# Performance work log

Hardware: AMD Instinct MI355X
Metric: run time of the kernel (lower is better)

The kernel has to match this reference:

```python
import jax, jax.numpy as jnp
import numpy as np

B, T, N = 8, 512, 64        # batch, seq_len, enc_in
E, H, P = 128, 256, 96      # embed_size, hidden_size, pred_len
LAMBDA = 0.001              # softshrink sparsity threshold
SCALE = 0.02


def _leaky(h):
    return jnp.where(h >= 0, h, 0.01 * h)


def _softshrink(y):
    return jnp.where(y > LAMBDA, y - LAMBDA, jnp.where(y < -LAMBDA, y + LAMBDA, jnp.zeros_like(y)))


def setup_inputs() -> dict:
    key = jax.random.key(0)
    ks = jax.random.split(key, 16)
    f32 = jnp.float32
    d = {
        "x": jax.random.normal(ks[0], (B, T, N), f32),
        "emb": jax.random.normal(ks[1], (1, E), f32),
        # MLP (embed_size -> hidden -> embed_size), stored as [in, out]
        "w1": SCALE * jax.random.normal(ks[2], (E, H), f32),
        "b1": SCALE * jax.random.normal(ks[3], (H,), f32),
        "w2": SCALE * jax.random.normal(ks[4], (H, E), f32),
        "b2": SCALE * jax.random.normal(ks[5], (E,), f32),
        # MLP_time (seq_len -> hidden -> seq_len)
        "tw1": SCALE * jax.random.normal(ks[6], (T, H), f32),
        "tb1": SCALE * jax.random.normal(ks[7], (H,), f32),
        "tw2": SCALE * jax.random.normal(ks[8], (H, T), f32),
        "tb2": SCALE * jax.random.normal(ks[9], (T,), f32),
        # fc (seq_len*embed -> hidden -> pred_len)
        "fw1": SCALE * jax.random.normal(ks[10], (T * E, H), f32),
        "fb1": SCALE * jax.random.normal(ks[11], (H,), f32),
        "fw2": SCALE * jax.random.normal(ks[12], (H, P), f32),
        "fb2": SCALE * jax.random.normal(ks[13], (P,), f32),
    }
    return d


def reference(x, emb, w1, b1, w2, b2, tw1, tb1, tw2, tb2, fw1, fb1, fw2, fb2):
    # x: [B, T, N]
    x_noD = jnp.transpose(x, (0, 2, 1))            # [B, N, T]
    xe = x_noD[..., None] * emb                    # tokenEmb -> [B, N, T, E]
    bias = xe + x_noD[..., None]

    # NorMLP_temporal: rfft over time, shared MLP on real/imag, softshrink, irfft
    xf = jnp.fft.rfft(xe, axis=2, norm="ortho")   # [B, N, T//2+1, E] complex64

    def mlp(z):
        return _leaky(z @ w1 + b1) @ w2 + b2

    yr = _softshrink(mlp(xf.real))
    yi = _softshrink(mlp(xf.imag))
    y = jax.lax.complex(yr, yi)
    xt = jnp.fft.irfft(y, n=T, axis=2, norm="ortho")  # [B, N, T, E]

    # NorMLP_temporal_WO_freq: MLP_time over last (time) dim of x_noD
    xn = _leaky(x_noD @ tw1 + tb1) @ tw2 + tb2        # [B, N, T]

    out = xt + xn[..., None] + bias                   # use_bias = 1

    flat = out.reshape(B, N, T * E)
    h = _leaky(flat @ fw1 + fb1) @ fw2 + fb2          # [B, N, P]
    return jnp.transpose(h, (0, 2, 1))                # [B, P, N]
```

## Files before the change

kernel.cpp:

```cpp
#include <hip/hip_runtime.h>
#include <hip/hip_bf16.h>


typedef unsigned int uint;
typedef unsigned short ushort_t;
typedef __attribute__((ext_vector_type(4))) float f32x4;
typedef __attribute__((ext_vector_type(8))) short short8;

#define LAMBDA_ 0.001f
#define RSQRT512 0.044194173824159220f

__device__ __forceinline__ ushort_t f2bf(float f) {
    uint u = __float_as_uint(f);
    uint r = (u + 0x7FFFu + ((u >> 16) & 1u)) >> 16;
    return (ushort_t)r;
}
__device__ __forceinline__ ushort_t f2bf_hw(float f) {
    union { __hip_bfloat16 h; ushort_t u; } c;
    c.h = __float2bfloat16(f);
    return c.u;
}
__device__ __forceinline__ float bf2f(ushort_t v) { return __uint_as_float(((uint)v) << 16); }
__device__ __forceinline__ float leaky_(float v) { return v >= 0.f ? v : 0.01f * v; }

__device__ __forceinline__ void gload_lds16(const ushort_t* g, ushort_t* l) {
    __builtin_amdgcn_global_load_lds((const __attribute__((address_space(1))) void*)g,
                                     (__attribute__((address_space(3))) void*)l, 16, 0, 0);
}

__global__ __launch_bounds__(256) void k_pre_plus(const float* __restrict__ x, const float* __restrict__ tw1,
                                                  const float* __restrict__ tw2, const float* __restrict__ fw1,
                                                  const float* __restrict__ emb, const float* __restrict__ w1,
                                                  const float* __restrict__ b1,
                                                  ushort_t* __restrict__ A1cat, ushort_t* __restrict__ B1cat,
                                                  ushort_t* __restrict__ Wt, ushort_t* __restrict__ tw2_bf,
                                                  ushort_t* __restrict__ fw1T,
                                                  float* __restrict__ u_g, int* __restrict__ idxs_g,
                                                  float* __restrict__ bpkey_g) {
    __shared__ float tile[64 * 65];
    __shared__ float key_s[256];
    __shared__ int idx_s[256];
    int bid = blockIdx.x;
    int tid = threadIdx.x;
    if (bid < 3072) {
        int region = bid >> 10;
        int id = ((bid & 1023) << 8) + tid;
        int a = id >> 9, c = id & 511;
        if (region == 0) {
            int f = (a <= 256) ? a : (a - 256);
            int m = (c * f) & 511;
            float ang = (float)m * (6.283185307179586f / 512.0f);
            float v = ((a <= 256) ? cosf(ang) : -sinf(ang)) * RSQRT512;
            ushort_t hi = f2bf(v);
            ushort_t lo = f2bf(v - bf2f(hi));
            size_t row = (size_t)a * 1536;
            B1cat[row + c] = hi;
            B1cat[row + 512 + c] = hi;
            B1cat[row + 1024 + c] = lo;
        } else if (region == 1) {
            int f = (a <= 256) ? a : (a - 256);
            int m = (c * f) & 511;
            float ang = (float)m * (6.283185307179586f / 512.0f);
            float v = ((a <= 256) ? cosf(ang) : -sinf(ang)) * RSQRT512;
            float sc = (a == 0 || a == 256) ? 1.0f : 2.0f;
            Wt[id] = f2bf(v * sc);
        } else {
            if ((bid & 1023) < 512) tw2_bf[id] = f2bf(tw2[id]);
        }
    } else if (bid < 3104) {
        int b = bid - 3072;
        int t0 = (b & 7) << 6, h0 = (b >> 3) << 6;
        float (*t64)[65] = (float(*)[65])tile;
        for (int i = 0; i < 16; ++i) {
            int idx = tid + i * 256;
            int r = idx >> 6, cc = idx & 63;
            t64[r][cc] = tw1[(size_t)(t0 + r) * 256 + h0 + cc];
        }
        __syncthreads();
        for (int i = 0; i < 16; ++i) {
            int idx = tid + i * 256;
            int rr = idx >> 6, cc2 = idx & 63;
            float v = t64[cc2][rr];
            ushort_t hi = f2bf(v);
            ushort_t lo = f2bf(v - bf2f(hi));
            size_t row = (size_t)(512 + h0 + rr) * 1536;
            int t = t0 + cc2;
            B1cat[row + t] = hi;
            B1cat[row + 512 + t] = hi;
            B1cat[row + 1024 + t] = lo;
        }
    } else if (bid < 3360) {
        int b = bid - 3104;
        int bb = b >> 5;
        int rem = b & 31;
        int t0 = (rem >> 1) << 5;
        int n0 = (rem & 1) << 5;
        int tx = tid & 31, ty = tid >> 5;
        float (*t32)[33] = (float(*)[33])tile;
        for (int i = 0; i < 4; ++i) {
            int tt = ty * 4 + i;
            t32[tt][tx] = x[(size_t)(bb * 512 + t0 + tt) * 64 + n0 + tx];
        }
        __syncthreads();
        for (int i = 0; i < 4; ++i) {
            int nn = ty * 4 + i;
            float v = t32[tx][nn];
            ushort_t hi = f2bf(v);
            ushort_t lo = f2bf(v - bf2f(hi));
            size_t row = (size_t)(bb * 64 + n0 + nn) * 1536;
            int t = t0 + tx;
            A1cat[row + t] = hi;
            A1cat[row + 512 + t] = lo;
            A1cat[row + 1024 + t] = hi;
        }
    } else if (bid < 7456) {
        int b = bid - 3360;
        int e  = b & 127;
        int hb = (b >> 7) & 3;
        int tt = b >> 9;
        int t0 = tt << 6, h0 = hb << 6;
        float (*t64)[65] = (float(*)[65])tile;
        for (int i = 0; i < 4; ++i) {
            int idx = tid + i * 256;
            int r = idx >> 4, c4 = idx & 15;
            const float* src = fw1 + ((size_t)(t0 + r) * 128 + e) * 256 + h0 + c4 * 4;
            float4 v = *(const float4*)src;
            t64[r][c4 * 4 + 0] = v.x;
            t64[r][c4 * 4 + 1] = v.y;
            t64[r][c4 * 4 + 2] = v.z;
            t64[r][c4 * 4 + 3] = v.w;
        }
        __syncthreads();
        for (int p = 0; p < 2; ++p) {
            int idx = tid + p * 256;
            int hh = idx >> 3, tg = idx & 7;
            short8 o;
            for (int j = 0; j < 8; ++j) o[j] = (short)f2bf(t64[tg * 8 + j][hh]);
            *(short8*)(fw1T + ((size_t)(h0 + hh) * 128 + e) * 512 + t0 + tg * 8) = o;
        }
    } else {
        float acc = 0.f;
#pragma unroll 8
        for (int e = 0; e < 128; ++e) acc += emb[e] * w1[e * 256 + tid];
        u_g[tid] = acc;
        float bb0 = b1[tid];
        key_s[tid] = (acc == 0.f) ? INFINITY : (-bb0 / acc);
        idx_s[tid] = tid;
        __syncthreads();
        for (int k = 2; k <= 256; k <<= 1) {
            for (int j = k >> 1; j > 0; j >>= 1) {
                int ixj = tid ^ j;
                if (ixj > tid) {
                    bool up = ((tid & k) == 0);
                    float a0 = key_s[tid], a1 = key_s[ixj];
                    if ((a0 > a1) == up) {
                        key_s[tid] = a1; key_s[ixj] = a0;
                        int t0 = idx_s[tid]; idx_s[tid] = idx_s[ixj]; idx_s[ixj] = t0;
                    }
                }
                __syncthreads();
            }
        }
        bpkey_g[tid] = key_s[tid];
        idxs_g[tid] = idx_s[tid];
    }
}

__global__ __launch_bounds__(256) void k_mid(const ushort_t* __restrict__ fw1T, const float* __restrict__ emb,
                                             const float* __restrict__ tb2,
                                             ushort_t* __restrict__ B1cat, ushort_t* __restrict__ F1sbf,
                                             float* __restrict__ p2v,
                                             const float* __restrict__ u_g, const float* __restrict__ b1,
                                             const float* __restrict__ w2, const float* __restrict__ b2,
                                             const int* __restrict__ idxs_g,
                                             ushort_t* __restrict__ Atab, ushort_t* __restrict__ Btab) {
    __shared__ float embs[128];
    __shared__ float red[256];
    __shared__ float sA[256], sB[256];
    int bid = blockIdx.x;
    int tid = threadIdx.x;
    if (bid < 256) {
        int h = bid;
        if (tid < 128) embs[tid] = 1.f + emb[tid];
        __syncthreads();
        int t2 = tid * 2;
        const ushort_t* base = fw1T + ((size_t)h << 16) + t2;
        float as0 = 0.f, as1 = 0.f, ae0 = 0.f, ae1 = 0.f;
#pragma unroll 4
        for (int e = 0; e < 128; ++e) {
            uint v = *(const uint*)(base + (size_t)e * 512);
            float v0 = bf2f((ushort_t)(v & 0xffff));
            float v1 = bf2f((ushort_t)(v >> 16));
            float w = embs[e];
            as0 += v0; as1 += v1;
            ae0 += w * v0; ae1 += w * v1;
        }
        *(uint*)(F1sbf + (size_t)h * 512 + t2) = (uint)f2bf(as0) | ((uint)f2bf(as1) << 16);
        ushort_t hi0 = f2bf(ae0), hi1 = f2bf(ae1);
        ushort_t lo0 = f2bf(ae0 - bf2f(hi0)), lo1 = f2bf(ae1 - bf2f(hi1));
        size_t row = (size_t)(768 + h) * 1536;
        uint hpk = (uint)hi0 | ((uint)hi1 << 16);
        *(uint*)(B1cat + row + t2) = hpk;
        *(uint*)(B1cat + row + 512 + t2) = hpk;
        *(uint*)(B1cat + row + 1024 + t2) = (uint)lo0 | ((uint)lo1 << 16);
        red[tid] = tb2[t2] * as0 + tb2[t2 + 1] * as1;
        __syncthreads();
        for (int off = 128; off > 0; off >>= 1) {
            if (tid < off) red[tid] += red[tid + off];
            __syncthreads();
        }
        if (tid == 0) p2v[h] = red[0];
    } else {
        int e = bid - 256, r = tid;
        float uu0 = u_g[r], bb0 = b1[r];
        float w0 = w2[r * 128 + e];
        float c = (uu0 < 0.f || (uu0 == 0.f && bb0 >= 0.f)) ? 1.0f : 0.01f;
        float bA = c * uu0 * w0, bB = c * bb0 * w0;
        int h = idxs_g[r];
        float uu = u_g[h], bb = b1[h];
        float w = w2[h * 128 + e];
        float sgn = (uu > 0.f) ? 0.99f : -0.99f;
        float dA = sgn * uu * w, dB = sgn * bb * w;
        sA[r] = bA; sB[r] = bB;
        __syncthreads();
        for (int off = 128; off > 0; off >>= 1) {
            if (r < off) { sA[r] += sA[r + off]; sB[r] += sB[r + off]; }
            __syncthreads();
        }
        float baseA = sA[0], baseB = sB[0] + b2[e];
        __syncthreads();
        sA[r] = dA; sB[r] = dB;
        __syncthreads();
        for (int off = 1; off < 256; off <<= 1) {
            float vA = (r >= off) ? sA[r - off] : 0.f;
            float vB = (r >= off) ? sB[r - off] : 0.f;
            __syncthreads();
            sA[r] += vA; sB[r] += vB;
            __syncthreads();
        }
        if (r == 0) { Atab[e] = f2bf(baseA); Btab[e] = f2bf(baseB); }
        Atab[(r + 1) * 128 + e] = f2bf(baseA + sA[r]);
        Btab[(r + 1) * 128 + e] = f2bf(baseB + sB[r]);
    }
}

__global__ __launch_bounds__(256) void k_g1p2(const ushort_t* __restrict__ A, const ushort_t* __restrict__ Bm,
                                              float* __restrict__ partialG,
                                              const ushort_t* __restrict__ tw2bf, const ushort_t* __restrict__ F1sbf,
                                              ushort_t* __restrict__ P2T) {
    __shared__ ushort_t As[128 * 72];
    __shared__ ushort_t Bs[128 * 72];
    int tid = threadIdx.x;
    int lane = tid & 63, wid = tid >> 6;
    int wr = wid >> 1, wc = wid & 1;
    int bid = blockIdx.x;
    f32x4 acc[4][4] = {};
    if (bid < 256) {
        int kch = bid & 7, tilei = bid >> 3;
        int nt = tilei & 7, mt = tilei >> 3;
        int m0 = mt * 128, n0 = nt * 128;
        for (int kt = 0; kt < 3; ++kt) {
            int kb = kch * 192 + kt * 64;
            __syncthreads();
            {
                uint4 va[4], vb[4];
                for (int i = 0; i < 4; ++i) {
                    int q = tid + i * 256;
                    int row = q >> 3, kcc = (q & 7) << 3;
                    va[i] = *(const uint4*)(A + (size_t)(m0 + row) * 1536 + kb + kcc);
                    vb[i] = *(const uint4*)(Bm + (size_t)(n0 + row) * 1536 + kb + kcc);
                }
                for (int i = 0; i < 4; ++i) {
                    int q = tid + i * 256;
                    int row = q >> 3, kcc = (q & 7) << 3;
                    *(uint4*)&As[row * 72 + kcc] = va[i];
                    *(uint4*)&Bs[row * 72 + kcc] = vb[i];
                }
            }
            __syncthreads();
            for (int ks = 0; ks < 2; ++ks) {
                short8 a[4], b[4];
                int kk = ks * 32 + (lane >> 4) * 8;
                for (int mi = 0; mi < 4; ++mi)
                    a[mi] = *(const short8*)&As[(wr * 64 + mi * 16 + (lane & 15)) * 72 + kk];
                for (int ni = 0; ni < 4; ++ni)
                    b[ni] = *(const short8*)&Bs[(wc * 64 + ni * 16 + (lane & 15)) * 72 + kk];
                for (int mi = 0; mi < 4; ++mi)
                    for (int ni = 0; ni < 4; ++ni)
                        acc[mi][ni] = __builtin_amdgcn_mfma_f32_16x16x32_bf16(a[mi], b[ni], acc[mi][ni], 0, 0, 0);
            }
        }
        float* pbase = partialG + (size_t)kch * 524288;
        int mb0 = m0 + wr * 64 + ((lane >> 4) << 2);
        int nb0 = n0 + wc * 64 + (lane & 15);
        for (int mi = 0; mi < 4; ++mi)
            for (int ni = 0; ni < 4; ++ni) {
                int mbase = mb0 + mi * 16;
                int n = nb0 + ni * 16;
                for (int r = 0; r < 4; ++r)
                    pbase[(size_t)(mbase + r) * 1024 + n] = acc[mi][ni][r];
            }
    } else {
        int b2i = bid - 256;
        int nt = b2i & 1, mt = b2i >> 1;
        int m0 = mt * 128, n0 = nt * 128;
        for (int kt = 0; kt < 8; ++kt) {
            int kb = kt * 64;
            __syncthreads();
            {
                uint4 va[4], vb[4];
                for (int i = 0; i < 4; ++i) {
                    int q = tid + i * 256;
                    int row = q >> 3, kcc = (q & 7) << 3;
                    va[i] = *(const uint4*)(tw2bf + (size_t)(m0 + row) * 512 + kb + kcc);
                    vb[i] = *(const uint4*)(F1sbf + (size_t)(n0 + row) * 512 + kb + kcc);
                }
                for (int i = 0; i < 4; ++i) {
                    int q = tid + i * 256;
                    int row = q >> 3, kcc = (q & 7) << 3;
                    *(uint4*)&As[row * 72 + kcc] = va[i];
                    *(uint4*)&Bs[row * 72 + kcc] = vb[i];
                }
            }
            __syncthreads();
            for (int ks = 0; ks < 2; ++ks) {
                short8 a[4], b[4];
                int kk = ks * 32 + (lane >> 4) * 8;
                for (int mi = 0; mi < 4; ++mi)
                    a[mi] = *(const short8*)&As[(wr * 64 + mi * 16 + (lane & 15)) * 72 + kk];
                for (int ni = 0; ni < 4; ++ni)
                    b[ni] = *(const short8*)&Bs[(wc * 64 + ni * 16 + (lane & 15)) * 72 + kk];
                for (int mi = 0; mi < 4; ++mi)
                    for (int ni = 0; ni < 4; ++ni)
                        acc[mi][ni] = __builtin_amdgcn_mfma_f32_16x16x32_bf16(a[mi], b[ni], acc[mi][ni], 0, 0, 0);
            }
        }
        int mb0 = m0 + wr * 64 + ((lane >> 4) << 2);
        int nb0 = n0 + wc * 64 + (lane & 15);
        for (int mi = 0; mi < 4; ++mi)
            for (int ni = 0; ni < 4; ++ni) {
                int mbase = mb0 + mi * 16;
                int n = nb0 + ni * 16;
                ushort4 o;
                o.x = f2bf(acc[mi][ni][0]);
                o.y = f2bf(acc[mi][ni][1]);
                o.z = f2bf(acc[mi][ni][2]);
                o.w = f2bf(acc[mi][ni][3]);
                *(ushort4*)(P2T + (size_t)n * 256 + mbase) = o;
            }
    }
}

__global__ __launch_bounds__(512) void k_gemm0r(const ushort_t* __restrict__ A, const ushort_t* __restrict__ Bm,
                                                ushort_t* __restrict__ M2T,
                                                const float* __restrict__ partialG, const float* __restrict__ tb1,
                                                float* __restrict__ s, ushort_t* __restrict__ hl,
                                                float* __restrict__ h2c) {
    __shared__ ushort_t As[2][128 * 64];
    __shared__ ushort_t Bs[2][128 * 64];
    int tid = threadIdx.x;
    int bid = blockIdx.x;
    if (bid >= 1024) {
        int id = (bid - 1024) * 512 + tid;
        int m = id >> 10, n = id & 1023;
        float acc = 0.f;
#pragma unroll
        for (int kc = 0; kc < 8; ++kc)
            acc += partialG[(size_t)kc * 524288 + id];
        if (n < 512) s[(size_t)m * 512 + n] = acc;
        else if (n < 768) hl[(size_t)m * 256 + (n - 512)] = f2bf(leaky_(acc + tb1[n - 512]));
        else h2c[(size_t)m * 256 + (n - 768)] = acc;
        return;
    }
    int lane = tid & 63, wid = tid >> 6;
    int wr = wid >> 2, wc = wid & 3;
    int xx = bid & 7, y = bid >> 3;
    int mt = y & 3;
    int nt = ((y >> 2) << 3) | xx;
    int m0 = mt * 128, n0 = nt * 128;
    int lrow = lane >> 3;
    int sg = (lane & 7) ^ lrow;
    auto issue = [&](int kt, int buf) {
        int kb = kt * 64;
        for (int i = 0; i < 2; ++i) {
            int rbase = wid * 16 + i * 8;
            gload_lds16(A + (size_t)(m0 + rbase + lrow) * 512 + kb + sg * 8, &As[buf][wid * 1024 + i * 512]);
            gload_lds16(Bm + (size_t)(n0 + rbase + lrow) * 512 + kb + sg * 8, &Bs[buf][wid * 1024 + i * 512]);
        }
    };
    f32x4 acc[4][2] = {};
    issue(0, 0);
    __syncthreads();
    int cur = 0;
    for (int kt = 0; kt < 8; ++kt) {
        int nxt = cur ^ 1;
        if (kt + 1 < 8) issue(kt + 1, nxt);
        __builtin_amdgcn_s_setprio(1);
        for (int ks = 0; ks < 2; ++ks) {
            short8 a[4], b[2];
            int sl = ks * 4 + (lane >> 4);
            for (int mi = 0; mi < 4; ++mi) {
                int row = wr * 64 + mi * 16 + (lane & 15);
                a[mi] = *(const short8*)&As[cur][row * 64 + ((sl ^ (row & 7)) << 3)];
            }
            for (int ni = 0; ni < 2; ++ni) {
                int row = wc * 32 + ni * 16 + (lane & 15);
                b[ni] = *(const short8*)&Bs[cur][row * 64 + ((sl ^ (row & 7)) << 3)];
            }
            for (int mi = 0; mi < 4; ++mi)
                for (int ni = 0; ni < 2; ++ni)
                    acc[mi][ni] = __builtin_amdgcn_mfma_f32_16x16x32_bf16(a[mi], b[ni], acc[mi][ni], 0, 0, 0);
        }
        __builtin_amdgcn_s_setprio(0);
        __syncthreads();
        cur = nxt;
    }
    ushort_t* cstage = &As[0][0];
    for (int mi = 0; mi < 4; ++mi) {
        int ml = wr * 64 + mi * 16 + ((lane >> 4) << 2);
        for (int ni = 0; ni < 2; ++ni) {
            int nl = wc * 32 + ni * 16 + (lane & 15);
            for (int r = 0; r < 4; ++r) {
                int row = ml + r;
                cstage[row * 128 + (nl ^ ((row & 7) << 4))] = f2bf(acc[mi][ni][r]);
            }
        }
    }
    __syncthreads();
    short8* d8 = (short8*)(M2T + ((size_t)(n0 >> 7) << 16) + (size_t)m0 * 128);
    for (int i = 0; i < 4; ++i) {
        int p = tid + i * 512;
        int row = p >> 4;
        int col0 = (p & 15) * 8;
        d8[p] = *(const short8*)&cstage[row * 128 + (col0 ^ ((row & 7) << 4))];
    }
}

__global__ __launch_bounds__(512) void k_gemm1(const float* __restrict__ s,
                                               const ushort_t* __restrict__ Atab, const ushort_t* __restrict__ Btab,
                                               const float* __restrict__ bpkey,
                                               const ushort_t* __restrict__ Bm,
                                               float* __restrict__ partial) {
    __shared__ ushort_t As[2][128 * 64];
    __shared__ ushort_t Bs[2][256 * 64];
    __shared__ float sv_s[1024];
    __shared__ ushort_t r_s[1024];
    __shared__ float bp_s[256];
    int tid = threadIdx.x;
    int lane = tid & 63, wid = tid >> 6;
    int wr = wid >> 2, wc = wid & 3;
    int bid = blockIdx.x;
    int xcd = bid & 7, j = bid >> 3;
    int kcl = j & 7, mt = j >> 3;
    int kc = xcd * 8 + kcl;
    int m0 = mt * 128;
    int k0 = kc * 1024;
    if (tid < 256) bp_s[tid] = bpkey[tid];
    __syncthreads();
    {
        int row = tid >> 2, j2 = (tid & 3) * 2;
        float2 sv2 = *(const float2*)(s + (size_t)(m0 + row) * 512 + kc * 8 + j2);
        float svv[2] = {sv2.x, sv2.y};
        for (int q = 0; q < 2; ++q) {
            float sv = svv[q];
            int lo = 0, hi = 256;
            while (lo < hi) { int mid = (lo + hi) >> 1; if (bp_s[mid] <= sv) lo = mid + 1; else hi = mid; }
            sv_s[row * 8 + j2 + q] = sv;
            r_s[row * 8 + j2 + q] = (ushort_t)lo;
        }
    }
    __syncthreads();

    int lrow = lane >> 3;
    int sg = (lane & 7) ^ lrow;
    auto issueB = [&](int kt, int buf) {
        int kb = k0 + kt * 64;
        for (int i = 0; i < 4; ++i) {
            int rbase = wid * 32 + i * 8;
            gload_lds16(Bm + (size_t)(rbase + lrow) * 65536 + kb + sg * 8, &Bs[buf][wid * 2048 + i * 512]);
        }
    };
    short8 ta[2], tb[2];
    float svr[2];
    auto gather = [&](int kt) {
        int kl = kt >> 1;
        for (int i = 0; i < 2; ++i) {
            int q = tid + i * 512;
            int row = q >> 3, slot = q & 7;
            int e0 = ((kt & 1) << 6) + slot * 8;
            int r = r_s[row * 8 + kl];
            svr[i] = sv_s[row * 8 + kl];
            ta[i] = *(const short8*)(Atab + r * 128 + e0);
            tb[i] = *(const short8*)(Btab + r * 128 + e0);
        }
    };
    auto cookwrite = [&](int buf) {
        for (int i = 0; i < 2; ++i) {
            int q = tid + i * 512;
            int row = q >> 3, slot = q & 7;
            float sv = svr[i];
            short8 o;
            for (int jj = 0; jj < 8; ++jj) {
                float y = fmaf(sv, bf2f((ushort_t)ta[i][jj]), bf2f((ushort_t)tb[i][jj]));
                y = y - fminf(fmaxf(y, -LAMBDA_), LAMBDA_);
                o[jj] = (short)f2bf_hw(y);
            }
            *(short8*)&As[buf][row * 64 + ((slot ^ (row & 7)) << 3)] = o;
        }
    };

    f32x4 acc[4][4] = {};
    issueB(0, 0);
    gather(0);
    cookwrite(0);
    __syncthreads();
    int cur = 0;
    for (int kt = 0; kt < 16; ++kt) {
        int nxt = cur ^ 1;
        if (kt + 1 < 16) { issueB(kt + 1, nxt); gather(kt + 1); }
        __builtin_amdgcn_s_setprio(1);
        for (int ks = 0; ks < 2; ++ks) {
            short8 a[4], b[4];
            int sl = ks * 4 + (lane >> 4);
            for (int mi = 0; mi < 4; ++mi) {
                int row = wr * 64 + mi * 16 + (lane & 15);
                a[mi] = *(const short8*)&As[cur][row * 64 + ((sl ^ (row & 7)) << 3)];
            }
            for (int ni = 0; ni < 4; ++ni) {
                int row = wc * 64 + ni * 16 + (lane & 15);
                b[ni] = *(const short8*)&Bs[cur][row * 64 + ((sl ^ (row & 7)) << 3)];
            }
            for (int mi = 0; mi < 4; ++mi)
                for (int ni = 0; ni < 4; ++ni)
                    acc[mi][ni] = __builtin_amdgcn_mfma_f32_16x16x32_bf16(a[mi], b[ni], acc[mi][ni], 0, 0, 0);
        }
        __builtin_amdgcn_s_setprio(0);
        if (kt + 1 < 16) cookwrite(nxt);
        __syncthreads();
        cur = nxt;
    }
    int mb0 = m0 + wr * 64 + ((lane >> 4) << 2);
    int nb0 = wc * 64 + (lane & 15);
    float* pbase = partial + (size_t)kc * 131072;
    for (int mi = 0; mi < 4; ++mi)
        for (int ni = 0; ni < 4; ++ni) {
            int mbase = mb0 + mi * 16;
            int n = nb0 + ni * 16;
            for (int r = 0; r < 4; ++r)
                pbase[(size_t)(mbase + r) * 256 + n] = acc[mi][ni][r];
        }
}

__global__ __launch_bounds__(128) void k_final(const float* __restrict__ partial, const ushort_t* __restrict__ hl,
                                               const ushort_t* __restrict__ P2T, const float* __restrict__ p2v,
                                               const float* __restrict__ h2c, const float* __restrict__ fb1,
                                               const float* __restrict__ fw2, const float* __restrict__ fb2,
                                               float* __restrict__ out) {
    __shared__ float a_s[256];
    __shared__ float hl_s[256];
    int bn = blockIdx.x;
    int tid = threadIdx.x;
    {
        uint v = *(const uint*)(hl + (size_t)bn * 256 + tid * 2);
        hl_s[tid * 2] = bf2f((ushort_t)(v & 0xffff));
        hl_s[tid * 2 + 1] = bf2f((ushort_t)(v >> 16));
    }
    __syncthreads();
    for (int p = 0; p < 2; ++p) {
        int i = tid + p * 128;
        float acc = p2v[i] + h2c[(size_t)bn * 256 + i] + fb1[i];
#pragma unroll 8
        for (int kc = 0; kc < 64; ++kc)
            acc += partial[((size_t)kc * 512 + bn) * 256 + i];
        const ushort_t* prow = P2T + (size_t)i * 256;
#pragma unroll 4
        for (int jb = 0; jb < 32; ++jb) {
            short8 pv = *(const short8*)(prow + jb * 8);
            for (int j8 = 0; j8 < 8; ++j8)
                acc += hl_s[jb * 8 + j8] * bf2f((ushort_t)pv[j8]);
        }
        a_s[i] = leaky_(acc);
    }
    __syncthreads();
    if (tid < 96) {
        float acc = fb2[tid];
        for (int hh = 0; hh < 256; ++hh)
            acc += a_s[hh] * fw2[hh * 96 + tid];
        int b = bn >> 6, n = bn & 63;
        out[(size_t)(b * 96 + tid) * 64 + n] = acc;
    }
}

extern "C" void kernel_launch(void* const* d_in, const int* in_sizes, int n_in,
                              void* d_out, int out_size, void* d_ws, size_t ws_size,
                              hipStream_t stream) {
    const float* x   = (const float*)d_in[0];
    const float* emb = (const float*)d_in[1];
    const float* w1  = (const float*)d_in[2];
    const float* b1  = (const float*)d_in[3];
    const float* w2  = (const float*)d_in[4];
    const float* b2  = (const float*)d_in[5];
    const float* tw1 = (const float*)d_in[6];
    const float* tb1 = (const float*)d_in[7];
    const float* tw2 = (const float*)d_in[8];
    const float* tb2 = (const float*)d_in[9];
    const float* fw1 = (const float*)d_in[10];
    const float* fb1 = (const float*)d_in[11];
    const float* fw2 = (const float*)d_in[12];
    const float* fb2 = (const float*)d_in[13];
    float* out = (float*)d_out;

    char* W = (char*)d_ws;
    size_t off = 0;
    auto take = [&](size_t bytes) { size_t r = off; off += (bytes + 255) & ~(size_t)255; return r; };
    ushort_t* fw1T  = (ushort_t*)(W + take(33554432));
    ushort_t* M2T   = (ushort_t*)(W + take(33554432));
    float* partial  = (float*)(W + take(64 * 512 * 256 * 4));
    float* partialG = (float*)(W + take(8 * 512 * 1024 * 4));
    ushort_t* A1cat = (ushort_t*)(W + take(512 * 1536 * 2));
    ushort_t* B1cat = (ushort_t*)(W + take(1024 * 1536 * 2));
    ushort_t* Wt    = (ushort_t*)(W + take(512 * 512 * 2));
    ushort_t* tw2bf = (ushort_t*)(W + take(256 * 512 * 2));
    ushort_t* F1sbf = (ushort_t*)(W + take(256 * 512 * 2));
    float* sbuf     = (float*)(W + take(512 * 512 * 4));
    ushort_t* hlbuf = (ushort_t*)(W + take(512 * 256 * 2));
    float* h2c      = (float*)(W + take(512 * 256 * 4));
    ushort_t* P2T   = (ushort_t*)(W + take(256 * 256 * 2));
    float* p2v      = (float*)(W + take(256 * 4));
    ushort_t* Atab  = (ushort_t*)(W + take(257 * 128 * 2));
    ushort_t* Btab  = (ushort_t*)(W + take(257 * 128 * 2));
    float* bpkey    = (float*)(W + take(256 * 4));
    float* u_g      = (float*)(W + take(256 * 4));
    int* idxs_g     = (int*)(W + take(256 * 4));
    (void)ws_size; (void)in_sizes; (void)n_in; (void)out_size;

    k_pre_plus<<<7457, 256, 0, stream>>>(x, tw1, tw2, fw1, emb, w1, b1,
                                         A1cat, B1cat, Wt, tw2bf, fw1T, u_g, idxs_g, bpkey);
    k_mid<<<384, 256, 0, stream>>>(fw1T, emb, tb2, B1cat, F1sbf, p2v,
                                   u_g, b1, w2, b2, idxs_g, Atab, Btab);
    k_g1p2<<<260, 256, 0, stream>>>(A1cat, B1cat, partialG, tw2bf, F1sbf, P2T);
    k_gemm0r<<<2048, 512, 0, stream>>>(Wt, fw1T, M2T, partialG, tb1, sbuf, hlbuf, h2c);
    k_gemm1<<<256, 512, 0, stream>>>(sbuf, Atab, Btab, bpkey, M2T, partial);
    k_final<<<512, 128, 0, stream>>>(partial, hlbuf, P2T, p2v, h2c, fb1, fw2, fb2, out);
}
```

Baseline: 141.3 us.

## Merge three GEMM stages into one launch and fold split-K reduction into consumers

Merges the two independent GEMM kernels (the M2T GEMM and the split-K/P2 GEMMs) into a single 512-thread launch that shares a double-buffered, swizzled global-to-LDS tile loop. The separate reduction pass that summed the 8 split-K partials into s, hl and h2c buffers is removed. That reduction now happens inside k_gemm1 and k_final, which read partialG directly. This saves one kernel launch, an intermediate round trip through memory and a serialization point. The cost is redundant partial-sum reads in the consumer kernels and smaller per-warp tiles for the split-K GEMMs.

```diff
diff --git a/kernel.cpp b/kernel.cpp
--- a/kernel.cpp
+++ b/kernel.cpp
@@ -26,6 +26,50 @@
 __device__ __forceinline__ void gload_lds16(const ushort_t* g, ushort_t* l) {
     __builtin_amdgcn_global_load_lds((const __attribute__((address_space(1))) void*)g,
                                      (__attribute__((address_space(3))) void*)l, 16, 0, 0);
+}
+
+__device__ __forceinline__ void tile_loop512(const ushort_t* __restrict__ A, int lda,
+                                             const ushort_t* __restrict__ Bm, int ldb,
+                                             int m0, int n0, int k0, int kIters,
+                                             f32x4 (&acc)[4][2],
+                                             ushort_t (&As)[2][128 * 64], ushort_t (&Bs)[2][128 * 64],
+                                             int tid, int lane, int wid, int wr, int wc) {
+    int lrow = lane >> 3;
+    int sg = (lane & 7) ^ lrow;
+    auto issue = [&](int kt, int buf) {
+        int kb = k0 + kt * 64;
+        for (int i = 0; i < 2; ++i) {
+            int rbase = wid * 16 + i * 8;
+            gload_lds16(A + (size_t)(m0 + rbase + lrow) * lda + kb + sg * 8, &As[buf][wid * 1024 + i * 512]);
+            gload_lds16(Bm + (size_t)(n0 + rbase + lrow) * ldb + kb + sg * 8, &Bs[buf][wid * 1024 + i * 512]);
+        }
+    };
+    issue(0, 0);
+    __syncthreads();
+    int cur = 0;
+    for (int kt = 0; kt < kIters; ++kt) {
+        int nxt = cur ^ 1;
+        if (kt + 1 < kIters) issue(kt + 1, nxt);
+        __builtin_amdgcn_s_setprio(1);
+        for (int ks = 0; ks < 2; ++ks) {
+            short8 a[4], b[2];
+            int sl = ks * 4 + (lane >> 4);
+            for (int mi = 0; mi < 4; ++mi) {
+                int row = wr * 64 + mi * 16 + (lane & 15);
+                a[mi] = *(const short8*)&As[cur][row * 64 + ((sl ^ (row & 7)) << 3)];
+            }
+            for (int ni = 0; ni < 2; ++ni) {
+                int row = wc * 32 + ni * 16 + (lane & 15);
+                b[ni] = *(const short8*)&Bs[cur][row * 64 + ((sl ^ (row & 7)) << 3)];
+            }
+            for (int mi = 0; mi < 4; ++mi)
+                for (int ni = 0; ni < 2; ++ni)
+                    acc[mi][ni] = __builtin_amdgcn_mfma_f32_16x16x32_bf16(a[mi], b[ni], acc[mi][ni], 0, 0, 0);
+        }
+        __builtin_amdgcn_s_setprio(0);
+        __syncthreads();
+        cur = nxt;
+    }
 }
 
 __global__ __launch_bounds__(256) void k_pre_plus(const float* __restrict__ x, const float* __restrict__ tw1,
@@ -244,101 +288,69 @@
     }
 }
 
-__global__ __launch_bounds__(256) void k_g1p2(const ushort_t* __restrict__ A, const ushort_t* __restrict__ Bm,
+__global__ __launch_bounds__(512) void k_big3(const ushort_t* __restrict__ Wt, const ushort_t* __restrict__ fw1T,
+                                              ushort_t* __restrict__ M2T,
+                                              const ushort_t* __restrict__ A1cat, const ushort_t* __restrict__ B1cat,
                                               float* __restrict__ partialG,
                                               const ushort_t* __restrict__ tw2bf, const ushort_t* __restrict__ F1sbf,
                                               ushort_t* __restrict__ P2T) {
-    __shared__ ushort_t As[128 * 72];
-    __shared__ ushort_t Bs[128 * 72];
+    __shared__ ushort_t As[2][128 * 64];
+    __shared__ ushort_t Bs[2][128 * 64];
     int tid = threadIdx.x;
     int lane = tid & 63, wid = tid >> 6;
-    int wr = wid >> 1, wc = wid & 1;
+    int wr = wid >> 2, wc = wid & 3;
     int bid = blockIdx.x;
-    f32x4 acc[4][4] = {};
-    if (bid < 256) {
-        int kch = bid & 7, tilei = bid >> 3;
+    f32x4 acc[4][2] = {};
+    if (bid < 1024) {
+        int xx = bid & 7, y = bid >> 3;
+        int mt = y & 3;
+        int nt = ((y >> 2) << 3) | xx;
+        int m0 = mt * 128, n0 = nt * 128;
+        tile_loop512(Wt, 512, fw1T, 512, m0, n0, 0, 8, acc, As, Bs, tid, lane, wid, wr, wc);
+        ushort_t* cstage = &As[0][0];
+        for (int mi = 0; mi < 4; ++mi) {
+            int ml = wr * 64 + mi * 16 + ((lane >> 4) << 2);
+            for (int ni = 0; ni < 2; ++ni) {
+                int nl = wc * 32 + ni * 16 + (lane & 15);
+                for (int r = 0; r < 4; ++r) {
+                    int row = ml + r;
+                    cstage[row * 128 + (nl ^ ((row & 7) << 4))] = f2bf(acc[mi][ni][r]);
+                }
+            }
+        }
+        __syncthreads();
+        short8* d8 = (short8*)(M2T + ((size_t)(n0 >> 7) << 16) + (size_t)m0 * 128);
+        for (int i = 0; i < 4; ++i) {
+            int p = tid + i * 512;
+            int row = p >> 4;
+            int col0 = (p & 15) * 8;
+            d8[p] = *(const short8*)&cstage[row * 128 + (col0 ^ ((row & 7) << 4))];
+        }
+    } else if (bid < 1280) {
+        int b = bid - 1024;
+        int kch = b & 7, tilei = b >> 3;
         int nt = tilei & 7, mt = tilei >> 3;
         int m0 = mt * 128, n0 = nt * 128;
-        for (int kt = 0; kt < 3; ++kt) {
-            int kb = kch * 192 + kt * 64;
-            __syncthreads();
-            {
-                uint4 va[4], vb[4];
-                for (int i = 0; i < 4; ++i) {
-                    int q = tid + i * 256;
-                    int row = q >> 3, kcc = (q & 7) << 3;
-                    va[i] = *(const uint4*)(A + (size_t)(m0 + row) * 1536 + kb + kcc);
-                    vb[i] = *(const uint4*)(Bm + (size_t)(n0 + row) * 1536 + kb + kcc);
-                }
-                for (int i = 0; i < 4; ++i) {
-                    int q = tid + i * 256;
-                    int row = q >> 3, kcc = (q & 7) << 3;
-                    *(uint4*)&As[row * 72 + kcc] = va[i];
-                    *(uint4*)&Bs[row * 72 + kcc] = vb[i];
-                }
-            }
-            __syncthreads();
-            for (int ks = 0; ks < 2; ++ks) {
-                short8 a[4], b[4];
-                int kk = ks * 32 + (lane >> 4) * 8;
-                for (int mi = 0; mi < 4; ++mi)
-                    a[mi] = *(const short8*)&As[(wr * 64 + mi * 16 + (lane & 15)) * 72 + kk];
-                for (int ni = 0; ni < 4; ++ni)
-                    b[ni] = *(const short8*)&Bs[(wc * 64 + ni * 16 + (lane & 15)) * 72 + kk];
-                for (int mi = 0; mi < 4; ++mi)
-                    for (int ni = 0; ni < 4; ++ni)
-                        acc[mi][ni] = __builtin_amdgcn_mfma_f32_16x16x32_bf16(a[mi], b[ni], acc[mi][ni], 0, 0, 0);
-            }
-        }
+        tile_loop512(A1cat, 1536, B1cat, 1536, m0, n0, kch * 192, 3, acc, As, Bs, tid, lane, wid, wr, wc);
         float* pbase = partialG + (size_t)kch * 524288;
         int mb0 = m0 + wr * 64 + ((lane >> 4) << 2);
-        int nb0 = n0 + wc * 64 + (lane & 15);
+        int nb0 = n0 + wc * 32 + (lane & 15);
         for (int mi = 0; mi < 4; ++mi)
-            for (int ni = 0; ni < 4; ++ni) {
+            for (int ni = 0; ni < 2; ++ni) {
                 int mbase = mb0 + mi * 16;
                 int n = nb0 + ni * 16;
                 for (int r = 0; r < 4; ++r)
                     pbase[(size_t)(mbase + r) * 1024 + n] = acc[mi][ni][r];
             }
     } else {
-        int b2i = bid - 256;
-        int nt = b2i & 1, mt = b2i >> 1;
+        int b = bid - 1280;
+        int nt = b & 1, mt = b >> 1;
         int m0 = mt * 128, n0 = nt * 128;
-        for (int kt = 0; kt < 8; ++kt) {
-            int kb = kt * 64;
-            __syncthreads();
-            {
-                uint4 va[4], vb[4];
-                for (int i = 0; i < 4; ++i) {
-                    int q = tid + i * 256;
-                    int row = q >> 3, kcc = (q & 7) << 3;
-                    va[i] = *(const uint4*)(tw2bf + (size_t)(m0 + row) * 512 + kb + kcc);
-                    vb[i] = *(const uint4*)(F1sbf + (size_t)(n0 + row) * 512 + kb + kcc);
-                }
-                for (int i = 0; i < 4; ++i) {
-                    int q = tid + i * 256;
-                    int row = q >> 3, kcc = (q & 7) << 3;
-                    *(uint4*)&As[row * 72 + kcc] = va[i];
-                    *(uint4*)&Bs[row * 72 + kcc] = vb[i];
-                }
-            }
-            __syncthreads();
-            for (int ks = 0; ks < 2; ++ks) {
-                short8 a[4], b[4];
-                int kk = ks * 32 + (lane >> 4) * 8;
-                for (int mi = 0; mi < 4; ++mi)
-                    a[mi] = *(const short8*)&As[(wr * 64 + mi * 16 + (lane & 15)) * 72 + kk];
-                for (int ni = 0; ni < 4; ++ni)
-                    b[ni] = *(const short8*)&Bs[(wc * 64 + ni * 16 + (lane & 15)) * 72 + kk];
-                for (int mi = 0; mi < 4; ++mi)
-                    for (int ni = 0; ni < 4; ++ni)
-                        acc[mi][ni] = __builtin_amdgcn_mfma_f32_16x16x32_bf16(a[mi], b[ni], acc[mi][ni], 0, 0, 0);
-            }
-        }
+        tile_loop512(tw2bf, 512, F1sbf, 512, m0, n0, 0, 8, acc, As, Bs, tid, lane, wid, wr, wc);
         int mb0 = m0 + wr * 64 + ((lane >> 4) << 2);
-        int nb0 = n0 + wc * 64 + (lane & 15);
+        int nb0 = n0 + wc * 32 + (lane & 15);
         for (int mi = 0; mi < 4; ++mi)
-            for (int ni = 0; ni < 4; ++ni) {
+            for (int ni = 0; ni < 2; ++ni) {
                 int mbase = mb0 + mi * 16;
                 int n = nb0 + ni * 16;
                 ushort4 o;
@@ -351,92 +363,7 @@
     }
 }
 
-__global__ __launch_bounds__(512) void k_gemm0r(const ushort_t* __restrict__ A, const ushort_t* __restrict__ Bm,
-                                                ushort_t* __restrict__ M2T,
-                                                const float* __restrict__ partialG, const float* __restrict__ tb1,
-                                                float* __restrict__ s, ushort_t* __restrict__ hl,
-                                                float* __restrict__ h2c) {
-    __shared__ ushort_t As[2][128 * 64];
-    __shared__ ushort_t Bs[2][128 * 64];
-    int tid = threadIdx.x;
-    int bid = blockIdx.x;
-    if (bid >= 1024) {
-        int id = (bid - 1024) * 512 + tid;
-        int m = id >> 10, n = id & 1023;
-        float acc = 0.f;
-#pragma unroll
-        for (int kc = 0; kc < 8; ++kc)
-            acc += partialG[(size_t)kc * 524288 + id];
-        if (n < 512) s[(size_t)m * 512 + n] = acc;
-        else if (n < 768) hl[(size_t)m * 256 + (n - 512)] = f2bf(leaky_(acc + tb1[n - 512]));
-        else h2c[(size_t)m * 256 + (n - 768)] = acc;
-        return;
-    }
-    int lane = tid & 63, wid = tid >> 6;
-    int wr = wid >> 2, wc = wid & 3;
-    int xx = bid & 7, y = bid >> 3;
-    int mt = y & 3;
-    int nt = ((y >> 2) << 3) | xx;
-    int m0 = mt * 128, n0 = nt * 128;
-    int lrow = lane >> 3;
-    int sg = (lane & 7) ^ lrow;
-    auto issue = [&](int kt, int buf) {
-        int kb = kt * 64;
-        for (int i = 0; i < 2; ++i) {
-            int rbase = wid * 16 + i * 8;
-            gload_lds16(A + (size_t)(m0 + rbase + lrow) * 512 + kb + sg * 8, &As[buf][wid * 1024 + i * 512]);
-            gload_lds16(Bm + (size_t)(n0 + rbase + lrow) * 512 + kb + sg * 8, &Bs[buf][wid * 1024 + i * 512]);
-        }
-    };
-    f32x4 acc[4][2] = {};
-    issue(0, 0);
-    __syncthreads();
-    int cur = 0;
-    for (int kt = 0; kt < 8; ++kt) {
-        int nxt = cur ^ 1;
-        if (kt + 1 < 8) issue(kt + 1, nxt);
-        __builtin_amdgcn_s_setprio(1);
-        for (int ks = 0; ks < 2; ++ks) {
-            short8 a[4], b[2];
-            int sl = ks * 4 + (lane >> 4);
-            for (int mi = 0; mi < 4; ++mi) {
-                int row = wr * 64 + mi * 16 + (lane & 15);
-                a[mi] = *(const short8*)&As[cur][row * 64 + ((sl ^ (row & 7)) << 3)];
-            }
-            for (int ni = 0; ni < 2; ++ni) {
-                int row = wc * 32 + ni * 16 + (lane & 15);
-                b[ni] = *(const short8*)&Bs[cur][row * 64 + ((sl ^ (row & 7)) << 3)];
-            }
-            for (int mi = 0; mi < 4; ++mi)
-                for (int ni = 0; ni < 2; ++ni)
-                    acc[mi][ni] = __builtin_amdgcn_mfma_f32_16x16x32_bf16(a[mi], b[ni], acc[mi][ni], 0, 0, 0);
-        }
-        __builtin_amdgcn_s_setprio(0);
-        __syncthreads();
-        cur = nxt;
-    }
-    ushort_t* cstage = &As[0][0];
-    for (int mi = 0; mi < 4; ++mi) {
-        int ml = wr * 64 + mi * 16 + ((lane >> 4) << 2);
-        for (int ni = 0; ni < 2; ++ni) {
-            int nl = wc * 32 + ni * 16 + (lane & 15);
-            for (int r = 0; r < 4; ++r) {
-                int row = ml + r;
-                cstage[row * 128 + (nl ^ ((row & 7) << 4))] = f2bf(acc[mi][ni][r]);
-            }
-        }
-    }
-    __syncthreads();
-    short8* d8 = (short8*)(M2T + ((size_t)(n0 >> 7) << 16) + (size_t)m0 * 128);
-    for (int i = 0; i < 4; ++i) {
-        int p = tid + i * 512;
-        int row = p >> 4;
-        int col0 = (p & 15) * 8;
-        d8[p] = *(const short8*)&cstage[row * 128 + (col0 ^ ((row & 7) << 4))];
-    }
-}
-
-__global__ __launch_bounds__(512) void k_gemm1(const float* __restrict__ s,
+__global__ __launch_bounds__(512) void k_gemm1(const float* __restrict__ partialG,
                                                const ushort_t* __restrict__ Atab, const ushort_t* __restrict__ Btab,
                                                const float* __restrict__ bpkey,
                                                const ushort_t* __restrict__ Bm,
@@ -459,10 +386,12 @@
     __syncthreads();
     {
         int row = tid >> 2, j2 = (tid & 3) * 2;
-        float2 sv2 = *(const float2*)(s + (size_t)(m0 + row) * 512 + kc * 8 + j2);
-        float svv[2] = {sv2.x, sv2.y};
+        const float* pg = partialG + (size_t)(m0 + row) * 1024 + kc * 8 + j2;
         for (int q = 0; q < 2; ++q) {
-            float sv = svv[q];
+            float sv = 0.f;
+#pragma unroll
+            for (int kch = 0; kch < 8; ++kch)
+                sv += pg[(size_t)kch * 524288 + q];
             int lo = 0, hi = 256;
             while (lo < hi) { int mid = (lo + hi) >> 1; if (bp_s[mid] <= sv) lo = mid + 1; else hi = mid; }
             sv_s[row * 8 + j2 + q] = sv;
@@ -551,24 +480,32 @@
         }
 }
 
-__global__ __launch_bounds__(128) void k_final(const float* __restrict__ partial, const ushort_t* __restrict__ hl,
+__global__ __launch_bounds__(128) void k_final(const float* __restrict__ partial, const float* __restrict__ partialG,
                                                const ushort_t* __restrict__ P2T, const float* __restrict__ p2v,
-                                               const float* __restrict__ h2c, const float* __restrict__ fb1,
+                                               const float* __restrict__ tb1, const float* __restrict__ fb1,
                                                const float* __restrict__ fw2, const float* __restrict__ fb2,
                                                float* __restrict__ out) {
     __shared__ float a_s[256];
     __shared__ float hl_s[256];
+    __shared__ float hc_s[256];
     int bn = blockIdx.x;
     int tid = threadIdx.x;
-    {
-        uint v = *(const uint*)(hl + (size_t)bn * 256 + tid * 2);
-        hl_s[tid * 2] = bf2f((ushort_t)(v & 0xffff));
-        hl_s[tid * 2 + 1] = bf2f((ushort_t)(v >> 16));
+    for (int q = 0; q < 2; ++q) {
+        int i = tid * 2 + q;
+        float a1 = 0.f, a2 = 0.f;
+#pragma unroll
+        for (int kch = 0; kch < 8; ++kch) {
+            const float* pg = partialG + (size_t)kch * 524288 + (size_t)bn * 1024;
+            a1 += pg[512 + i];
+            a2 += pg[768 + i];
+        }
+        hl_s[i] = leaky_(a1 + tb1[i]);
+        hc_s[i] = a2;
     }
     __syncthreads();
     for (int p = 0; p < 2; ++p) {
         int i = tid + p * 128;
-        float acc = p2v[i] + h2c[(size_t)bn * 256 + i] + fb1[i];
+        float acc = p2v[i] + hc_s[i] + fb1[i];
 #pragma unroll 8
         for (int kc = 0; kc < 64; ++kc)
             acc += partial[((size_t)kc * 512 + bn) * 256 + i];
@@ -622,9 +559,6 @@
     ushort_t* Wt    = (ushort_t*)(W + take(512 * 512 * 2));
     ushort_t* tw2bf = (ushort_t*)(W + take(256 * 512 * 2));
     ushort_t* F1sbf = (ushort_t*)(W + take(256 * 512 * 2));
-    float* sbuf     = (float*)(W + take(512 * 512 * 4));
-    ushort_t* hlbuf = (ushort_t*)(W + take(512 * 256 * 2));
-    float* h2c      = (float*)(W + take(512 * 256 * 4));
     ushort_t* P2T   = (ushort_t*)(W + take(256 * 256 * 2));
     float* p2v      = (float*)(W + take(256 * 4));
     ushort_t* Atab  = (ushort_t*)(W + take(257 * 128 * 2));
@@ -638,8 +572,7 @@
                                          A1cat, B1cat, Wt, tw2bf, fw1T, u_g, idxs_g, bpkey);
     k_mid<<<384, 256, 0, stream>>>(fw1T, emb, tb2, B1cat, F1sbf, p2v,
                                    u_g, b1, w2, b2, idxs_g, Atab, Btab);
-    k_g1p2<<<260, 256, 0, stream>>>(A1cat, B1cat, partialG, tw2bf, F1sbf, P2T);
-    k_gemm0r<<<2048, 512, 0, stream>>>(Wt, fw1T, M2T, partialG, tb1, sbuf, hlbuf, h2c);
-    k_gemm1<<<256, 512, 0, stream>>>(sbuf, Atab, Btab, bpkey, M2T, partial);
-    k_final<<<512, 128, 0, stream>>>(partial, hlbuf, P2T, p2v, h2c, fb1, fw2, fb2, out);
-}
+    k_big3<<<1284, 512, 0, stream>>>(Wt, fw1T, M2T, A1cat, B1cat, partialG, tw2bf, F1sbf, P2T);
+    k_gemm1<<<256, 512, 0, stream>>>(partialG, Atab, Btab, bpkey, M2T, partial);
+    k_final<<<512, 128, 0, stream>>>(partial, partialG, P2T, p2v, tb1, fb1, fw2, fb2, out);
+}
```

Result: faster. 137.4 us (-2.8%).
